# Kernel optimization log

Hardware: AMD Instinct MI355X
Metric: run time of the kernel (lower is better)

The kernel has to match this reference:

```python
import jax, jax.numpy as jnp
import numpy as np

ARCH = (1024, 2048, 2048, 512)
STEPS = 20
LR = 0.1
BATCH = 4096


def setup_inputs() -> dict:
    key = jax.random.key(0)
    ks = jax.random.split(key, 1 + len(ARCH) - 1)
    x = jax.random.normal(ks[0], (BATCH, ARCH[0]), dtype=jnp.float32)
    inp = {"x": x}
    # forward layers: weight (out, in) as in torch nn.Linear, orthogonal-ish init gain sqrt(2)
    for i in range(len(ARCH) - 1):
        fan_in = ARCH[i]
        W = jax.random.normal(ks[1 + i], (ARCH[i + 1], fan_in), dtype=jnp.float32) * jnp.sqrt(2.0 / fan_in)
        inp[f"W{i}"] = W
        inp[f"b{i}"] = jnp.zeros((ARCH[i + 1],), dtype=jnp.float32)
    return inp


def _errors(r, Ws):
    # errors[-1] = r[-1]; errors[i] = r[i] - tanh(F.linear(r[i+1], W_i.T)) = r[i] - tanh(r[i+1] @ W_i)
    errs = [None] * len(ARCH)
    errs[-1] = r[-1]
    for i in range(len(Ws) - 1, -1, -1):
        errs[i] = r[i] - jnp.tanh(r[i + 1] @ Ws[i])  # (B, arch[i])
    return errs


def _pc_forward(x, Ws, bs):
    # initialize states with a no-grad feedforward pass (torch.no_grad -> stop_gradient)
    r = [x]
    t = x
    for W, b in zip(Ws, bs):
        t = jnp.tanh(t @ W.T + b)
        r.append(jax.lax.stop_gradient(t))

    def step(carry, _):
        r = list(carry)
        errs = _errors(r, Ws)
        new_r = [r[0]]  # r[0] = x, fixed
        for i in range(1, len(ARCH)):
            feedback = errs[i - 1] @ Ws[i - 1].T  # F.linear(errors[i-1], W)
            new_r.append(r[i] + LR * (-errs[i] + feedback))
        return tuple(new_r), None

    r, _ = jax.lax.scan(step, tuple(r), None, length=STEPS)
    r = list(r)
    final_errs = _errors(r, Ws)
    total_error = 0.5 * sum(jnp.sum(e * e) for e in final_errs)
    return r[-1], total_error


def reference(x, W0, b0, W1, b1, W2, b2):
    Ws = [W0, W1, W2]
    bs = [b0, b1, b2]
    return _pc_forward(x, Ws, bs)
```

## Files before the change

### kernel.cpp

```cpp
#include <hip/hip_runtime.h>

typedef unsigned short u16;
typedef __bf16 bf16_t;
typedef bf16_t bf16x8 __attribute__((ext_vector_type(8)));
typedef u16 u16x8 __attribute__((ext_vector_type(8)));
typedef float f32x4 __attribute__((ext_vector_type(4)));

__device__ __forceinline__ u16 f2bf(float f) {
    unsigned u = __builtin_bit_cast(unsigned, f);
    u += 0x7fffu + ((u >> 16) & 1u);
    return (u16)(u >> 16);
}
__device__ __forceinline__ float bf2f(u16 h) {
    unsigned u = ((unsigned)h) << 16;
    return __builtin_bit_cast(float, u);
}
__device__ __forceinline__ float fast_tanh(float x) {
    x = fminf(fmaxf(x, -20.f), 20.f);
    float e = __expf(2.f * x);
    return (e - 1.f) * __builtin_amdgcn_rcpf(e + 1.f);
}
__device__ __forceinline__ void gload_lds16(const void* g, void* l) {
    __builtin_amdgcn_global_load_lds((__attribute__((address_space(1))) void*)(g),
                                     (__attribute__((address_space(3))) void*)(l),
                                     16, 0, 0);
}
__device__ __forceinline__ bf16x8 ld8(const u16* p) {
    return __builtin_bit_cast(bf16x8, *(const u16x8*)p);
}

#define VMW0() __builtin_amdgcn_s_waitcnt(0x3F70)
#define MEMFENCE() asm volatile("" ::: "memory")
#define SCHED0() __builtin_amdgcn_sched_barrier(0)



__global__ void cvt_bf16(const float* __restrict__ src, u16* __restrict__ dst, int n4) {
    int i = blockIdx.x * blockDim.x + threadIdx.x;
    if (i < n4) {
        float4 v = ((const float4*)src)[i];
        ushort4 o;
        o.x = f2bf(v.x); o.y = f2bf(v.y); o.z = f2bf(v.z); o.w = f2bf(v.w);
        ((ushort4*)dst)[i] = o;
    }
}

__global__ void transpose_cvt(const float* __restrict__ W, u16* __restrict__ WT, int R, int C) {
    __shared__ float tile[32][33];
    int c0 = blockIdx.x * 32, r0 = blockIdx.y * 32;
    int tx = threadIdx.x & 31, ty = threadIdx.x >> 5;
#pragma unroll
    for (int i = 0; i < 32; i += 8)
        tile[ty + i][tx] = W[(size_t)(r0 + ty + i) * C + (c0 + tx)];
    __syncthreads();
#pragma unroll
    for (int i = 0; i < 32; i += 8)
        WT[(size_t)(c0 + ty + i) * R + (r0 + tx)] = f2bf(tile[tx][ty + i]);
}

__global__ void blockify(const u16* __restrict__ src, u16* __restrict__ dst, int K) {
    const int nk = K >> 5;
    const int rb = blockIdx.x / nk, cb = blockIdx.x % nk;
    const int t = threadIdx.x;
    const int kloc = (t & 7) * 4;
    u16* d = dst + (size_t)blockIdx.x * 4096 + ((kloc >> 3) << 10) + (kloc & 7);
    const u16* s = src + (size_t)(rb * 128) * K + cb * 32 + kloc;
#pragma unroll
    for (int p = 0; p < 4; ++p) {
        int row = (t >> 3) + p * 32;
        *(ushort4*)(d + row * 8) = *(const ushort4*)(s + (size_t)row * K);
    }
}


struct Seg {
    const u16* A; const u16* B;
    const u16* rsrcb;
    const float* rsrcf;
    const float* bias;
    const u16* esub;
    float* outf;
    u16* outbf;
    int K, N, blkStart, mode, accum;
};
struct Phase {
    Seg seg[3];
    int bEnd0, bEnd1;
};

#define ISSUE_A(dst, kk, mh) do { \
    const u16* _p = SH + buf * 16384 + (wr2 + (kk)) * 4096 + aoff + (mh) * 512; \
    dst[0] = ld8(_p); dst[1] = ld8(_p + 128); dst[2] = ld8(_p + 256); dst[3] = ld8(_p + 384); \
} while (0)

#define ISSUE_B(dst, kk) do { \
    const u16* _p = SH + 32768 + buf * 16384 + (wch2 + (kk)) * 4096 + boff; \
    dst[0] = ld8(_p); dst[1] = ld8(_p + 128); dst[2] = ld8(_p + 256); dst[3] = ld8(_p + 384); \
} while (0)

#define MFMACL(mh, A_, B_) do { \
    __builtin_amdgcn_s_setprio(1); \
    _Pragma("unroll") \
    for (int _i = 0; _i < 4; ++_i) { \
        _Pragma("unroll") \
        for (int _n = 0; _n < 4; ++_n) \
            acc[(mh) * 4 + _i][_n] = __builtin_amdgcn_mfma_f32_16x16x32_bf16( \
                A_[_i], B_[_n], acc[(mh) * 4 + _i][_n], 0, 0, 0); \
    } \
    __builtin_amdgcn_s_setprio(0); \
} while (0)

__global__ __launch_bounds__(512, 2) void pc_phase(Phase ph, float* __restrict__ errAcc) {
    __shared__ __align__(16) u16 SH[65536];
    __shared__ float red[8];

    const int bid = blockIdx.x;
    const int segi = (bid >= ph.bEnd0 ? 1 : 0) + (bid >= ph.bEnd1 ? 1 : 0);

    const u16* Ab = ph.seg[segi].A;
    const u16* Bb = ph.seg[segi].B;
    const int K = ph.seg[segi].K;
    const int local = bid - ph.seg[segi].blkStart;
    const int bx2 = local >> 4;
    const int by2 = local & 15;
    const int nk32 = K >> 5, NT = K >> 6;

    const int tid  = threadIdx.x;
    const int wave = tid >> 6, lane = tid & 63;
    const int q    = lane >> 4, ln = lane & 15;
    const int wr = wave >> 2, wc = wave & 3;
    const int wr2 = wr * 2, wch2 = (wc >> 1) * 2;
    const int aoff = q * 1024 + ln * 8;
    const int boff = q * 1024 + ((wc & 1) * 64 + ln) * 8;

    const size_t t8 = (size_t)tid * 8;
    const u16* gA0 = Ab + ((size_t)(by2 * 2 + 0) * nk32) * 4096 + t8;
    const u16* gA1 = Ab + ((size_t)(by2 * 2 + 1) * nk32) * 4096 + t8;
    const u16* gB0 = Bb + ((size_t)(bx2 * 2 + 0) * nk32) * 4096 + t8;
    const u16* gB1 = Bb + ((size_t)(bx2 * 2 + 1) * nk32) * 4096 + t8;
    const int wb = wave * 512;

    auto stageA = [&](int cb, int bf, int ks) {
        const size_t g = (size_t)cb * 4096;
        u16* a = SH + bf * 16384 + ks * 4096 + wb;
        gload_lds16(gA0 + g, a);
        gload_lds16(gA1 + g, a + 8192);
    };
    auto stageB = [&](int cb, int bf, int ks) {
        const size_t g = (size_t)cb * 4096;
        u16* b = SH + 32768 + bf * 16384 + ks * 4096 + wb;
        gload_lds16(gB0 + g, b);
        gload_lds16(gB1 + g, b + 8192);
    };

    f32x4 acc[8][4];
#pragma unroll
    for (int i = 0; i < 8; ++i)
#pragma unroll
        for (int j = 0; j < 4; ++j)
            acc[i][j] = (f32x4){0.f, 0.f, 0.f, 0.f};

    stageA(0, 0, 0); stageB(0, 0, 0);
    stageA(1, 0, 1); stageB(1, 0, 1);

    bf16x8 aRe[4], aRo[4], bR[4];

    for (int t = 0; t < NT; ++t) {
        const int buf = t & 1, nbuf = buf ^ 1;
        const int more = (t + 1 < NT);
        VMW0();
        MEMFENCE(); __builtin_amdgcn_s_barrier(); MEMFENCE();

        ISSUE_B(bR, 0); ISSUE_A(aRe, 0, 0); SCHED0();
        if (more) { stageA(2 * t + 2, nbuf, 0); stageB(2 * t + 2, nbuf, 0); }
        ISSUE_A(aRo, 0, 1); SCHED0();
        MFMACL(0, aRe, bR); SCHED0();
        if (more) { stageA(2 * t + 3, nbuf, 1); stageB(2 * t + 3, nbuf, 1); }
        ISSUE_A(aRe, 1, 0); SCHED0();
        MFMACL(1, aRo, bR); SCHED0();
        ISSUE_B(bR, 1); ISSUE_A(aRo, 1, 1); SCHED0();
        MFMACL(0, aRe, bR); SCHED0();
        MFMACL(1, aRo, bR);
    }
    __syncthreads();

    const int N = ph.seg[segi].N;
    const int mode = ph.seg[segi].mode;
    const int accum = ph.seg[segi].accum;
    const u16* rsrcbP = ph.seg[segi].rsrcb;
    const float* rsrcfP = ph.seg[segi].rsrcf;
    const float* biasP = ph.seg[segi].bias;
    const u16* esubP = ph.seg[segi].esub;
    float* outfP = ph.seg[segi].outf;
    u16* outbfP = ph.seg[segi].outbf;

    const int nb32 = N >> 5;
    const size_t regOff = ((size_t)(by2 * 2 + wr) * nb32 + (size_t)(bx2 * 2 + (wc >> 1)) * 4) * 4096;
    u16* SLICE = SH + wave * 8192;

    float lsum = 0.f;
    const int rowg0 = by2 * 256 + wr * 128 + q * 4;
    const int colg0 = bx2 * 256 + wc * 64;

#pragma unroll
    for (int ct = 0; ct < 2; ++ct) {
        const size_t tileOff = regOff + (size_t)((wc & 1) * 2 + ct) * 4096;
        if (mode == 1 || mode == 2) {
#pragma unroll
            for (int p = 0; p < 8; ++p)
                *(u16x8*)(SLICE + p * 512 + lane * 8) =
                    *(const u16x8*)(rsrcbP + tileOff + p * 512 + lane * 8);
        }
        if (mode == 2) {
#pragma unroll
            for (int p = 0; p < 8; ++p)
                *(u16x8*)(SLICE + 4096 + p * 512 + lane * 8) =
                    *(const u16x8*)(esubP + tileOff + p * 512 + lane * 8);
        }
#pragma unroll
        for (int nh = 0; nh < 2; ++nh) {
            const int nt = ct * 2 + nh;
            const int ci = nh * 16 + ln;
            const int co = ((ci >> 3) & 3) * 1024 + (ci & 7);
            const int colg = colg0 + nt * 16 + ln;
            const float bnt = (mode == 0) ? biasP[colg] : 0.f;
#pragma unroll
            for (int mt = 0; mt < 8; ++mt) {
#pragma unroll
                for (int r = 0; r < 4; ++r) {
                    const int row = mt * 16 + q * 4 + r;
                    const int o = co + row * 8;
                    const float c = acc[mt][nt][r];
                    float v;
                    if (mode == 0) {
                        v = fast_tanh(c + bnt);
                        if (outfP) outfP[(size_t)(rowg0 + mt * 16 + r) * N + colg] = v;
                    } else if (mode == 1) {
                        v = bf2f(SLICE[o]) - fast_tanh(c);
                        if (accum) lsum += v * v;
                    } else if (mode == 2) {
                        v = bf2f(SLICE[o]) + 0.1f * (c - bf2f(SLICE[4096 + o]));
                    } else {
                        const size_t idx = (size_t)(rowg0 + mt * 16 + r) * N + colg;
                        v = 0.9f * rsrcfP[idx] + 0.1f * c;
                        outfP[idx] = v;
                        if (accum) lsum += v * v;
                    }
                    SLICE[o] = f2bf(v);
                }
            }
        }
#pragma unroll
        for (int p = 0; p < 8; ++p)
            *(u16x8*)(outbfP + tileOff + p * 512 + lane * 8) =
                *(const u16x8*)(SLICE + p * 512 + lane * 8);
    }

    if (accum) {
        lsum *= 0.5f;
#pragma unroll
        for (int o = 32; o > 0; o >>= 1) lsum += __shfl_down(lsum, o);
        if (lane == 0) red[wave] = lsum;
        __syncthreads();
        if (tid == 0) {
            float s = 0.f;
#pragma unroll
            for (int i = 0; i < 8; ++i) s += red[i];
            atomicAdd(errAcc, s);
        }
    }
}


extern "C" void kernel_launch(void* const* d_in, const int* in_sizes, int n_in,
                              void* d_out, int out_size, void* d_ws, size_t ws_size,
                              hipStream_t stream) {
    const float* x  = (const float*)d_in[0];
    const float* W0 = (const float*)d_in[1];
    const float* b0 = (const float*)d_in[2];
    const float* W1 = (const float*)d_in[3];
    const float* b1 = (const float*)d_in[4];
    const float* W2 = (const float*)d_in[5];
    const float* b2 = (const float*)d_in[6];

    const int Bz = 4096;

    char* ws = (char*)d_ws;
    size_t off = 0;
    auto alloc = [&](size_t bytes) -> char* {
        char* p = ws + off;
        off += (bytes + 255) & ~(size_t)255;
        return p;
    };

    u16*   r1b = (u16*)  alloc((size_t)Bz * 2048 * 2);
    u16*   r2b = (u16*)  alloc((size_t)Bz * 2048 * 2);
    u16*   r3b = (u16*)  alloc((size_t)Bz * 512 * 2);
    u16*   e0b = (u16*)  alloc((size_t)Bz * 1024 * 2);
    u16*   e1b = (u16*)  alloc((size_t)Bz * 2048 * 2);
    u16*   e2b = (u16*)  alloc((size_t)Bz * 2048 * 2);
    u16*   xb  = (u16*)  alloc((size_t)Bz * 1024 * 2);
    u16*   W0b = (u16*)  alloc((size_t)2048 * 1024 * 2);
    u16*   W0t = (u16*)  alloc((size_t)1024 * 2048 * 2);
    u16*   W1b = (u16*)  alloc((size_t)2048 * 2048 * 2);
    u16*   W1t = (u16*)  alloc((size_t)2048 * 2048 * 2);
    u16*   W2b = (u16*)  alloc((size_t)512 * 2048 * 2);
    u16*   W2t = (u16*)  alloc((size_t)2048 * 512 * 2);
    u16*   tmp = (u16*)  alloc((size_t)2048 * 2048 * 2);

    float* r3f    = (float*)d_out;
    float* errAcc = ((float*)d_out) + (size_t)Bz * 512;

    auto blkify = [&](const u16* s, u16* d, int M, int K) {
        blockify<<<(M / 128) * (K / 32), 256, 0, stream>>>(s, d, K);
    };

    cvt_bf16<<<(Bz * 1024 / 4) / 256, 256, 0, stream>>>(x, tmp, Bz * 1024 / 4);
    blkify(tmp, xb, Bz, 1024);
    cvt_bf16<<<(2048 * 1024 / 4) / 256, 256, 0, stream>>>(W0, tmp, 2048 * 1024 / 4);
    blkify(tmp, W0b, 2048, 1024);
    cvt_bf16<<<(2048 * 2048 / 4) / 256, 256, 0, stream>>>(W1, tmp, 2048 * 2048 / 4);
    blkify(tmp, W1b, 2048, 2048);
    cvt_bf16<<<(512 * 2048 / 4) / 256, 256, 0, stream>>>(W2, tmp, 512 * 2048 / 4);
    blkify(tmp, W2b, 512, 2048);
    transpose_cvt<<<dim3(1024 / 32, 2048 / 32), 256, 0, stream>>>(W0, tmp, 2048, 1024);
    blkify(tmp, W0t, 1024, 2048);
    transpose_cvt<<<dim3(2048 / 32, 2048 / 32), 256, 0, stream>>>(W1, tmp, 2048, 2048);
    blkify(tmp, W1t, 2048, 2048);
    transpose_cvt<<<dim3(2048 / 32, 512 / 32),  256, 0, stream>>>(W2, tmp, 512, 2048);
    blkify(tmp, W2t, 2048, 512);

    hipMemsetAsync(errAcc, 0, 4, stream);

    auto mkseg = [&](const u16* A, const u16* B, int K, int N,
                     const u16* rsrcb, const float* rsrcf, const float* bias,
                     const u16* esub, float* outf, u16* outbf,
                     int mode, int accum) {
        Seg s;
        s.A = A; s.B = B; s.rsrcb = rsrcb; s.rsrcf = rsrcf; s.bias = bias;
        s.esub = esub; s.outf = outf; s.outbf = outbf;
        s.K = K; s.N = N; s.blkStart = 0; s.mode = mode; s.accum = accum;
        return s;
    };
    auto nblk = [&](int N) { return (N / 256) * (Bz / 256); };

    auto launch1 = [&](Seg s0) {
        Phase ph;
        int b0c = nblk(s0.N);
        ph.seg[0] = s0; ph.seg[1] = s0; ph.seg[2] = s0;
        ph.bEnd0 = b0c; ph.bEnd1 = b0c;
        pc_phase<<<b0c, 512, 0, stream>>>(ph, errAcc);
    };
    auto launch3 = [&](Seg s0, Seg s1, Seg s2) {
        Phase ph;
        int b0c = nblk(s0.N), b1c = nblk(s1.N), b2c = nblk(s2.N);
        s1.blkStart = b0c; s2.blkStart = b0c + b1c;
        ph.seg[0] = s0; ph.seg[1] = s1; ph.seg[2] = s2;
        ph.bEnd0 = b0c; ph.bEnd1 = b0c + b1c;
        pc_phase<<<b0c + b1c + b2c, 512, 0, stream>>>(ph, errAcc);
    };

    launch1(mkseg(xb,  W0b, 1024, 2048, nullptr, nullptr, b0, nullptr, nullptr, r1b, 0, 0));
    launch1(mkseg(r1b, W1b, 2048, 2048, nullptr, nullptr, b1, nullptr, nullptr, r2b, 0, 0));
    launch1(mkseg(r2b, W2b, 2048, 512,  nullptr, nullptr, b2, nullptr, r3f,     r3b, 0, 0));

    for (int s = 0; s < 20; ++s) {
        int last = (s == 19) ? 1 : 0;
        launch3(mkseg(r2b, W1t, 2048, 2048, r1b, nullptr, nullptr, nullptr, nullptr, e1b, 1, 0),
                mkseg(r1b, W0t, 2048, 1024, xb,  nullptr, nullptr, nullptr, nullptr, e0b, 1, 0),
                mkseg(r3b, W2t, 512,  2048, r2b, nullptr, nullptr, nullptr, nullptr, e2b, 1, 0));
        launch3(mkseg(e1b, W1b, 2048, 2048, r2b, nullptr, nullptr, e2b, nullptr, r2b, 2, 0),
                mkseg(e2b, W2b, 2048, 512,  nullptr, r3f, nullptr, nullptr, r3f,  r3b, 3, last),
                mkseg(e0b, W0b, 1024, 2048, r1b, nullptr, nullptr, e1b, nullptr, r1b, 2, 0));
    }

    launch3(mkseg(r2b, W1t, 2048, 2048, r1b, nullptr, nullptr, nullptr, nullptr, e1b, 1, 1),
            mkseg(r1b, W0t, 2048, 1024, xb,  nullptr, nullptr, nullptr, nullptr, e0b, 1, 1),
            mkseg(r3b, W2t, 512,  2048, r2b, nullptr, nullptr, nullptr, nullptr, e2b, 1, 1));
}
```

Measured before the change: 4.053 ms.

## Restructure GEMM main loop into per-k-slice barriers with partial waitcnts

Reworks the GEMM main loop's software pipeline. Each k-slice now issues all LDS reads for that slice, then prefetches the next global-to-LDS stage, gates on lgkmcnt(4) after a barrier, and waits on vmcnt(4) instead of draining all global loads. The loop also closes each half-iteration with its own barrier. The aim is to overlap global prefetch with MFMA work and cut the full vmcnt(0) stall per iteration, at the cost of an extra barrier per iteration and fragile hand-tuned wait counts.

New measurement: 3.662 ms. 9.6% less time.

```diff
diff --git a/kernel.cpp b/kernel.cpp
--- a/kernel.cpp
+++ b/kernel.cpp
@@ -29,9 +29,24 @@
     return __builtin_bit_cast(bf16x8, *(const u16x8*)p);
 }
 
+#define VMW4() __builtin_amdgcn_s_waitcnt(0x3F74)
 #define VMW0() __builtin_amdgcn_s_waitcnt(0x3F70)
 #define MEMFENCE() asm volatile("" ::: "memory")
 #define SCHED0() __builtin_amdgcn_sched_barrier(0)
+
+#define GATE4() do { \
+    MEMFENCE(); __builtin_amdgcn_s_barrier(); \
+    asm volatile("s_waitcnt lgkmcnt(4)" ::: "memory"); \
+    SCHED0(); \
+} while (0)
+#define LGKM0() do { \
+    asm volatile("s_waitcnt lgkmcnt(0)" ::: "memory"); \
+    SCHED0(); \
+} while (0)
+#define CLOSE() do { \
+    SCHED0(); \
+    MEMFENCE(); __builtin_amdgcn_s_barrier(); MEMFENCE(); \
+} while (0)
 
 
 
@@ -162,25 +177,32 @@
 
     stageA(0, 0, 0); stageB(0, 0, 0);
     stageA(1, 0, 1); stageB(1, 0, 1);
+    VMW4();
+    MEMFENCE(); __builtin_amdgcn_s_barrier(); MEMFENCE();
 
     bf16x8 aRe[4], aRo[4], bR[4];
 
     for (int t = 0; t < NT; ++t) {
         const int buf = t & 1, nbuf = buf ^ 1;
         const int more = (t + 1 < NT);
-        VMW0();
-        MEMFENCE(); __builtin_amdgcn_s_barrier(); MEMFENCE();
-
-        ISSUE_B(bR, 0); ISSUE_A(aRe, 0, 0); SCHED0();
+
+        ISSUE_B(bR, 0); ISSUE_A(aRe, 0, 0); ISSUE_A(aRo, 0, 1);
         if (more) { stageA(2 * t + 2, nbuf, 0); stageB(2 * t + 2, nbuf, 0); }
-        ISSUE_A(aRo, 0, 1); SCHED0();
-        MFMACL(0, aRe, bR); SCHED0();
+        GATE4();
+        MFMACL(0, aRe, bR);
+        LGKM0();
+        MFMACL(1, aRo, bR);
+        if (more) VMW4(); else VMW0();
+        CLOSE();
+
+        ISSUE_B(bR, 1); ISSUE_A(aRe, 1, 0); ISSUE_A(aRo, 1, 1);
         if (more) { stageA(2 * t + 3, nbuf, 1); stageB(2 * t + 3, nbuf, 1); }
-        ISSUE_A(aRe, 1, 0); SCHED0();
-        MFMACL(1, aRo, bR); SCHED0();
-        ISSUE_B(bR, 1); ISSUE_A(aRo, 1, 1); SCHED0();
-        MFMACL(0, aRe, bR); SCHED0();
+        GATE4();
+        MFMACL(0, aRe, bR);
+        LGKM0();
         MFMACL(1, aRo, bR);
+        if (more) VMW4();
+        CLOSE();
     }
     __syncthreads();
 
```

## Software-pipeline GEMM main loop with partial waits and split barriers

Applied to the files above, without the earlier changes.

Restructures the double-buffered MFMA main loop so LDS fragment reads for the next sub-step are issued before the current MFMA block. Global-to-LDS staging is interleaved at finer granularity, using partial vmcnt and lgkmcnt waits instead of a full drain and one barrier per iteration. The goal is to hide LDS and global load latency behind MFMA work. The cost is an extra barrier per iteration, more live fragment registers, and more delicate ordering of waits that could race if the counts are wrong.

Result: faster. 3.676 ms (-9.3%).

```diff
diff --git a/kernel.cpp b/kernel.cpp
--- a/kernel.cpp
+++ b/kernel.cpp
@@ -29,9 +29,15 @@
     return __builtin_bit_cast(bf16x8, *(const u16x8*)p);
 }
 
+#define VMW4() __builtin_amdgcn_s_waitcnt(0x3F74)
+#define VMW2() __builtin_amdgcn_s_waitcnt(0x3F72)
 #define VMW0() __builtin_amdgcn_s_waitcnt(0x3F70)
 #define MEMFENCE() asm volatile("" ::: "memory")
 #define SCHED0() __builtin_amdgcn_sched_barrier(0)
+#define SBAR() do { MEMFENCE(); __builtin_amdgcn_s_barrier(); MEMFENCE(); } while (0)
+#define LGKM4() do { asm volatile("s_waitcnt lgkmcnt(4)" ::: "memory"); SCHED0(); } while (0)
+#define LGKM8() do { asm volatile("s_waitcnt lgkmcnt(8)" ::: "memory"); SCHED0(); } while (0)
+#define LGKM0() do { asm volatile("s_waitcnt lgkmcnt(0)" ::: "memory"); SCHED0(); } while (0)
 
 
 
@@ -88,13 +94,13 @@
     int bEnd0, bEnd1;
 };
 
-#define ISSUE_A(dst, kk, mh) do { \
-    const u16* _p = SH + buf * 16384 + (wr2 + (kk)) * 4096 + aoff + (mh) * 512; \
+#define RD_A(dst, bufi, kk, mh) do { \
+    const u16* _p = SH + (bufi) * 16384 + (wr2 + (kk)) * 4096 + aoff + (mh) * 512; \
     dst[0] = ld8(_p); dst[1] = ld8(_p + 128); dst[2] = ld8(_p + 256); dst[3] = ld8(_p + 384); \
 } while (0)
 
-#define ISSUE_B(dst, kk) do { \
-    const u16* _p = SH + 32768 + buf * 16384 + (wch2 + (kk)) * 4096 + boff; \
+#define RD_B(dst, bufi, kk) do { \
+    const u16* _p = SH + 32768 + (bufi) * 16384 + (wch2 + (kk)) * 4096 + boff; \
     dst[0] = ld8(_p); dst[1] = ld8(_p + 128); dst[2] = ld8(_p + 256); dst[3] = ld8(_p + 384); \
 } while (0)
 
@@ -108,6 +114,7 @@
                 A_[_i], B_[_n], acc[(mh) * 4 + _i][_n], 0, 0, 0); \
     } \
     __builtin_amdgcn_s_setprio(0); \
+    SCHED0(); \
 } while (0)
 
 __global__ __launch_bounds__(512, 2) void pc_phase(Phase ph, float* __restrict__ errAcc) {
@@ -162,25 +169,46 @@
 
     stageA(0, 0, 0); stageB(0, 0, 0);
     stageA(1, 0, 1); stageB(1, 0, 1);
-
-    bf16x8 aRe[4], aRo[4], bR[4];
+    VMW4();
+    SBAR();
+
+    bf16x8 Ae[4], Ao[4], Bc[4], Bn[4];
+    RD_B(Bc, 0, 0);
+    RD_A(Ae, 0, 0, 0);
 
     for (int t = 0; t < NT; ++t) {
         const int buf = t & 1, nbuf = buf ^ 1;
         const int more = (t + 1 < NT);
-        VMW0();
-        MEMFENCE(); __builtin_amdgcn_s_barrier(); MEMFENCE();
-
-        ISSUE_B(bR, 0); ISSUE_A(aRe, 0, 0); SCHED0();
-        if (more) { stageA(2 * t + 2, nbuf, 0); stageB(2 * t + 2, nbuf, 0); }
-        ISSUE_A(aRo, 0, 1); SCHED0();
-        MFMACL(0, aRe, bR); SCHED0();
-        if (more) { stageA(2 * t + 3, nbuf, 1); stageB(2 * t + 3, nbuf, 1); }
-        ISSUE_A(aRe, 1, 0); SCHED0();
-        MFMACL(1, aRo, bR); SCHED0();
-        ISSUE_B(bR, 1); ISSUE_A(aRo, 1, 1); SCHED0();
-        MFMACL(0, aRe, bR); SCHED0();
-        MFMACL(1, aRo, bR);
+
+        RD_A(Ao, buf, 0, 1);
+        if (more) stageA(2 * t + 2, nbuf, 0);
+        LGKM4();
+        MFMACL(0, Ae, Bc);
+
+        if (more) VMW2(); else VMW0();
+        SBAR();
+        RD_B(Bn, buf, 1);
+        RD_A(Ae, buf, 1, 0);
+        if (more) stageB(2 * t + 2, nbuf, 0);
+        LGKM8();
+        MFMACL(1, Ao, Bc);
+
+        RD_A(Ao, buf, 1, 1);
+        if (more) stageA(2 * t + 3, nbuf, 1);
+        LGKM4();
+        MFMACL(0, Ae, Bn);
+
+        if (more) {
+            stageB(2 * t + 3, nbuf, 1);
+            VMW4();
+            SBAR();
+            RD_B(Bc, nbuf, 0);
+            RD_A(Ae, nbuf, 0, 0);
+            LGKM8();
+        } else {
+            LGKM0();
+        }
+        MFMACL(1, Ao, Bn);
     }
     __syncthreads();
 
```
